# Kernel tuning notes

Measured on AMD Instinct MI355X. Metric: run time of the kernel, lower is better.

Reference implementation:

```python
import jax, jax.numpy as jnp
import numpy as np

T, B, C, H = 2048, 4, 1024, 16
DK = C // H
CLAMP = 1e8  # fp32 clamp bound used by the original module


def setup_inputs() -> dict:
    key = jax.random.key(0)
    ks = jax.random.split(key, 12)
    s = 1.0 / np.sqrt(C)
    inp = {
        'query': jax.random.normal(ks[0], (T, B, C), jnp.float32),
        'key': jax.random.normal(ks[1], (T, B, C), jnp.float32),
        'value': jax.random.normal(ks[2], (T, B, C), jnp.float32),
        'key_padding_mask': jax.random.randint(ks[3], (B, T), 0, 2) > 0,
        # nn.Linear params, stored torch-style as [out, in]
        'Wq': jax.random.uniform(ks[4], (C, C), jnp.float32, -s, s),
        'bq': jax.random.uniform(ks[5], (C,), jnp.float32, -s, s),
        'Wk': jax.random.uniform(ks[6], (C, C), jnp.float32, -s, s),
        'bk': jax.random.uniform(ks[7], (C,), jnp.float32, -s, s),
        'Wv': jax.random.uniform(ks[8], (C, C), jnp.float32, -s, s),
        'bv': jax.random.uniform(ks[9], (C,), jnp.float32, -s, s),
        'Wo': jax.random.uniform(ks[10], (C, C), jnp.float32, -s, s),
        'bo': jax.random.uniform(ks[11], (C,), jnp.float32, -s, s),
    }
    return inp


def _attn(query, key, value, key_padding_mask, Wq, bq, Wk, bk, Wv, bv, Wo, bo):
    # T x B x C -> B x T x C
    q_in = jnp.swapaxes(query, 0, 1)
    k_in = jnp.swapaxes(key, 0, 1)
    v_in = jnp.swapaxes(value, 0, 1)
    b = q_in.shape[0]
    # projections (torch Linear: x @ W.T + b), split heads -> B x H x T x dk
    q = (q_in @ Wq.T + bq).reshape(b, -1, H, DK).transpose(0, 2, 1, 3)
    k = (k_in @ Wk.T + bk).reshape(b, -1, H, DK).transpose(0, 2, 1, 3)
    v = (v_in @ Wv.T + bv).reshape(b, -1, H, DK).transpose(0, 2, 1, 3)
    scores = jnp.einsum('bhqd,bhkd->bhqk', q, k) / np.sqrt(DK)
    if key_padding_mask is not None:
        scores = jnp.where(key_padding_mask[:, None, None, :], -jnp.inf, scores)
    scores = jnp.clip(scores, -CLAMP, CLAMP)
    attn = jax.nn.softmax(scores.astype(jnp.float32), axis=-1).astype(scores.dtype)
    # dropout is identity in eval mode
    x = jnp.einsum('bhqk,bhkd->bhqd', attn, v)
    x = x.transpose(0, 2, 1, 3).reshape(b, -1, H * DK)
    out = x @ Wo.T + bo
    return jnp.swapaxes(out, 0, 1)  # back to T x B x C


def reference(query, key, value, key_padding_mask, Wq, bq, Wk, bk, Wv, bv, Wo, bo):
    return _attn(query, key, value, key_padding_mask, Wq, bq, Wk, bk, Wv, bv, Wo, bo)
```

## Files before the change

kernel.cpp:

```cpp
#include <hip/hip_runtime.h>
#include <hip/hip_bf16.h>
#include <cstddef>
#include <cstdint>

constexpr int T  = 2048;
constexpr int B  = 4;
constexpr int C  = 1024;
constexpr int H  = 16;
constexpr int DK = 64;
constexpr int M  = T * B;

typedef __attribute__((ext_vector_type(8))) short bf16x8;
typedef __attribute__((ext_vector_type(4))) float f32x4;
typedef __attribute__((ext_vector_type(4))) unsigned short u16x4;
typedef __attribute__((ext_vector_type(8))) unsigned short u16x8;

__device__ inline unsigned short f2bf(float f) {
    union { float f; uint32_t u; } v; v.f = f;
    uint32_t u = v.u + 0x7fff + ((v.u >> 16) & 1);
    return (unsigned short)(u >> 16);
}
__device__ inline float bf2f(unsigned short h) {
    union { uint32_t u; float f; } v; v.u = (uint32_t)h << 16;
    return v.f;
}
__device__ inline uint32_t cvtpk_bf16(float lo, float hi) {
    uint32_t r;
    asm("v_cvt_pk_bf16_f32 %0, %1, %2" : "=v"(r) : "v"(lo), "v"(hi));
    return r;
}

__device__ inline void gload_lds16(const void* g, void* l) {
    auto gp = reinterpret_cast<const __attribute__((address_space(1))) char*>(
        reinterpret_cast<uintptr_t>(g));
    auto lp = reinterpret_cast<__attribute__((address_space(3))) char*>(
        reinterpret_cast<uintptr_t>(l));
    __builtin_amdgcn_global_load_lds(gp, lp, 16, 0, 0);
}

__global__ __launch_bounds__(256) void convert_in(const float* __restrict__ q,
                                                  const float* __restrict__ k,
                                                  const float* __restrict__ v,
                                                  unsigned short* __restrict__ dq,
                                                  unsigned short* __restrict__ dk2,
                                                  unsigned short* __restrict__ dv) {
    const float* s; unsigned short* d;
    if (blockIdx.y == 0) { s = q; d = dq; }
    else if (blockIdx.y == 1) { s = k; d = dk2; }
    else { s = v; d = dv; }
    const size_t i = ((size_t)blockIdx.x * 256 + threadIdx.x) * 8;
    const float4 a = *(const float4*)(s + i);
    const float4 b = *(const float4*)(s + i + 4);
    u16x8 o;
    o[0] = f2bf(a.x); o[1] = f2bf(a.y); o[2] = f2bf(a.z); o[3] = f2bf(a.w);
    o[4] = f2bf(b.x); o[5] = f2bf(b.y); o[6] = f2bf(b.z); o[7] = f2bf(b.w);
    *(u16x8*)(d + i) = o;
}

__global__ __launch_bounds__(256) void convert_w(const float* __restrict__ wq,
                                                 const float* __restrict__ wk,
                                                 const float* __restrict__ wv,
                                                 unsigned short* __restrict__ dst) {
    const float* s = blockIdx.y == 0 ? wq : (blockIdx.y == 1 ? wk : wv);
    unsigned short* d = dst + (size_t)blockIdx.y * C * C;
    const size_t i = ((size_t)blockIdx.x * 256 + threadIdx.x) * 8;
    const float4 a = *(const float4*)(s + i);
    const float4 b = *(const float4*)(s + i + 4);
    u16x8 o;
    o[0] = f2bf(a.x); o[1] = f2bf(a.y); o[2] = f2bf(a.z); o[3] = f2bf(a.w);
    o[4] = f2bf(b.x); o[5] = f2bf(b.y); o[6] = f2bf(b.z); o[7] = f2bf(b.w);
    *(u16x8*)(d + i) = o;
}

__global__ __launch_bounds__(256) void convert_wo(const float* __restrict__ wo,
                                                  unsigned short* __restrict__ hi,
                                                  unsigned short* __restrict__ lo) {
    const size_t i = ((size_t)blockIdx.x * 256 + threadIdx.x) * 8;
#pragma unroll
    for (int j = 0; j < 8; j++) {
        const float x = wo[i + j];
        const unsigned short h = f2bf(x);
        hi[i + j] = h;
        lo[i + j] = f2bf(x - bf2f(h));
    }
}

__global__ __launch_bounds__(256) void qkv_gemm(
        const unsigned short* __restrict__ Aq,
        const unsigned short* __restrict__ Ak,
        const unsigned short* __restrict__ Av,
        const unsigned short* __restrict__ W,
        const float* __restrict__ bq, const float* __restrict__ bk,
        const float* __restrict__ bv,
        unsigned short* __restrict__ Qb, unsigned short* __restrict__ Kb,
        unsigned short* __restrict__ Vb) {
    __shared__ __align__(16) unsigned short As[128][32];
    __shared__ __align__(16) unsigned short Ws[128][32];

    const int tid = threadIdx.x;
    const int m0 = blockIdx.x * 128;
    const int n0 = blockIdx.y * 128;
    const int w = tid >> 6, lane = tid & 63;
    const int g = lane >> 4, c16 = lane & 15;
    const int wr = (w >> 1) * 64, wc = (w & 1) * 64;

    const int which = n0 >> 10;
    const unsigned short* A = which == 0 ? Aq : (which == 1 ? Ak : Av);

    f32x4 acc[4][4] = {};

    for (int k0 = 0; k0 < C; k0 += 32) {
        __syncthreads();
#pragma unroll
        for (int half = 0; half < 2; half++) {
            const int chunk = tid + half * 256;
            const int r = chunk >> 2, s = chunk & 3;
            gload_lds16(A + (size_t)(m0 + r) * C + k0 + s * 8,
                        (char*)&As[0][0] + chunk * 16);
            gload_lds16(W + (size_t)(n0 + r) * C + k0 + s * 8,
                        (char*)&Ws[0][0] + chunk * 16);
        }
        __syncthreads();

        bf16x8 af[4], bfr[4];
#pragma unroll
        for (int mf = 0; mf < 4; mf++)
            af[mf] = *(const bf16x8*)&As[wr + mf * 16 + c16][g * 8];
#pragma unroll
        for (int nf = 0; nf < 4; nf++)
            bfr[nf] = *(const bf16x8*)&Ws[wc + nf * 16 + c16][g * 8];
#pragma unroll
        for (int mf = 0; mf < 4; mf++)
#pragma unroll
            for (int nf = 0; nf < 4; nf++)
                acc[mf][nf] = __builtin_amdgcn_mfma_f32_16x16x32_bf16(
                    af[mf], bfr[nf], acc[mf][nf], 0, 0, 0);
    }

    unsigned short* dst = which == 0 ? Qb : (which == 1 ? Kb : Vb);
    const float* bias = which == 0 ? bq : (which == 1 ? bk : bv);
    const float scale = which == 0 ? 0.180336889f : 1.0f;

#pragma unroll
    for (int mf = 0; mf < 4; mf++) {
#pragma unroll
        for (int nf = 0; nf < 4; nf++) {
            const int n = n0 + wc + nf * 16 + c16;
            const int c = n & 1023;
            const int hh = c >> 6, dk = c & 63;
            const float bval = bias[c];
#pragma unroll
            for (int r = 0; r < 4; r++) {
                const int m = m0 + wr + mf * 16 + g * 4 + r;
                const int t = m >> 2, bb = m & 3;
                dst[((size_t)(bb * H + hh) * T + t) * DK + dk] =
                    f2bf((acc[mf][nf][r] + bval) * scale);
            }
        }
    }
}

__global__ __launch_bounds__(256) void oproj_gemm(
        const unsigned short* __restrict__ Xh, const unsigned short* __restrict__ Xl,
        const unsigned short* __restrict__ Wh, const unsigned short* __restrict__ Wl,
        const float* __restrict__ bo, float* __restrict__ out) {
    __shared__ __align__(16) unsigned short Ahs[128][32];
    __shared__ __align__(16) unsigned short Als[128][32];
    __shared__ __align__(16) unsigned short Bhs[128][32];
    __shared__ __align__(16) unsigned short Bls[128][32];

    const int tid = threadIdx.x;
    const int m0 = blockIdx.x * 128;
    const int n0 = blockIdx.y * 128;
    const int w = tid >> 6, lane = tid & 63;
    const int g = lane >> 4, c16 = lane & 15;
    const int wr = (w >> 1) * 64, wc = (w & 1) * 64;

    f32x4 acc[4][4] = {};

    for (int k0 = 0; k0 < C; k0 += 32) {
        __syncthreads();
#pragma unroll
        for (int half = 0; half < 2; half++) {
            const int chunk = tid + half * 256;
            const int r = chunk >> 2, s = chunk & 3;
            const size_t goffA = (size_t)(m0 + r) * C + k0 + s * 8;
            const size_t goffB = (size_t)(n0 + r) * C + k0 + s * 8;
            gload_lds16(Xh + goffA, (char*)&Ahs[0][0] + chunk * 16);
            gload_lds16(Xl + goffA, (char*)&Als[0][0] + chunk * 16);
            gload_lds16(Wh + goffB, (char*)&Bhs[0][0] + chunk * 16);
            gload_lds16(Wl + goffB, (char*)&Bls[0][0] + chunk * 16);
        }
        __syncthreads();

        bf16x8 ah[4], al[4];
#pragma unroll
        for (int mf = 0; mf < 4; mf++) {
            ah[mf] = *(const bf16x8*)&Ahs[wr + mf * 16 + c16][g * 8];
            al[mf] = *(const bf16x8*)&Als[wr + mf * 16 + c16][g * 8];
        }
#pragma unroll
        for (int nf = 0; nf < 4; nf++) {
            const bf16x8 wh = *(const bf16x8*)&Bhs[wc + nf * 16 + c16][g * 8];
            const bf16x8 wl = *(const bf16x8*)&Bls[wc + nf * 16 + c16][g * 8];
#pragma unroll
            for (int mf = 0; mf < 4; mf++) {
                acc[mf][nf] = __builtin_amdgcn_mfma_f32_16x16x32_bf16(ah[mf], wh, acc[mf][nf], 0, 0, 0);
                acc[mf][nf] = __builtin_amdgcn_mfma_f32_16x16x32_bf16(al[mf], wh, acc[mf][nf], 0, 0, 0);
                acc[mf][nf] = __builtin_amdgcn_mfma_f32_16x16x32_bf16(ah[mf], wl, acc[mf][nf], 0, 0, 0);
            }
        }
    }

#pragma unroll
    for (int mf = 0; mf < 4; mf++) {
#pragma unroll
        for (int nf = 0; nf < 4; nf++) {
            const int n = n0 + wc + nf * 16 + c16;
            const float bval = bo[n];
#pragma unroll
            for (int r = 0; r < 4; r++) {
                const int m = m0 + wr + mf * 16 + g * 4 + r;
                const int t = m & 2047, bb = m >> 11;
                out[((size_t)t * B + bb) * C + n] = acc[mf][nf][r] + bval;
            }
        }
    }
}

__global__ __launch_bounds__(256) void attn_mfma(const unsigned short* __restrict__ Q,
                                                 const unsigned short* __restrict__ K,
                                                 const unsigned short* __restrict__ V,
                                                 const int* __restrict__ mask,
                                                 unsigned short* __restrict__ Xh,
                                                 unsigned short* __restrict__ Xl) {
    __shared__ __align__(16) short Ks[64][72];
    __shared__ __align__(16) short Vt[64][72];
    __shared__ __align__(16) short Pl[4][16][72];

    const int b = blockIdx.z, h = blockIdx.y;
    const int q0 = blockIdx.x * 128;
    const int tid = threadIdx.x;
    const int wl = tid >> 6;
    const int lane = tid & 63;
    const int g = lane >> 4;
    const int c16 = lane & 15;

    const size_t bh = (size_t)(b * H + h) * T * DK;
    const unsigned short* Qg = Q + bh;
    const unsigned short* Kg = K + bh;
    const unsigned short* Vg = V + bh;
    const int* mb = mask + b * T;

    bf16x8 qf[2][2];
#pragma unroll
    for (int qs = 0; qs < 2; qs++)
#pragma unroll
        for (int sl = 0; sl < 2; sl++)
            qf[qs][sl] = *(const bf16x8*)(Qg +
                (size_t)(q0 + wl * 32 + qs * 16 + c16) * DK + g * 8 + sl * 32);

    f32x4 o[2][4] = {};
    float lrow[2] = {0.0f, 0.0f};

    for (int kt = 0; kt < T / 64; ++kt) {
        const int kv0 = kt * 64;
        __syncthreads();

#pragma unroll
        for (int i = 0; i < 2; i++) {
            const int chunk = tid + i * 256;
            const int r = chunk >> 3, cc = chunk & 7;
            *(uint4*)&Ks[r][cc * 8] =
                *(const uint4*)(Kg + (size_t)(kv0 + r) * DK + cc * 8);
        }
        {
            const int kp = tid & 31, dc = tid >> 5;
            const u16x8 a0 = *(const u16x8*)(Vg + (size_t)(kv0 + 2 * kp) * DK + dc * 8);
            const u16x8 a1 = *(const u16x8*)(Vg + (size_t)(kv0 + 2 * kp + 1) * DK + dc * 8);
#pragma unroll
            for (int j = 0; j < 8; j++) {
                const uint32_t pk = (uint32_t)a0[j] | ((uint32_t)a1[j] << 16);
                *(uint32_t*)&Vt[dc * 8 + j][2 * kp] = pk;
            }
        }
        __syncthreads();

        const unsigned long long mbits = __ballot(mb[kv0 + lane] != 0);

        bf16x8 kf[4][2], vf[4][2];
#pragma unroll
        for (int t = 0; t < 4; t++)
#pragma unroll
            for (int sl = 0; sl < 2; sl++) {
                kf[t][sl] = *(const bf16x8*)&Ks[t * 16 + c16][g * 8 + sl * 32];
                vf[t][sl] = *(const bf16x8*)&Vt[t * 16 + c16][g * 8 + sl * 32];
            }

#pragma unroll
        for (int qs = 0; qs < 2; qs++) {
            f32x4 s4[4];
#pragma unroll
            for (int t = 0; t < 4; t++) {
                f32x4 acc = {0.f, 0.f, 0.f, 0.f};
#pragma unroll
                for (int sl = 0; sl < 2; sl++)
                    acc = __builtin_amdgcn_mfma_f32_16x16x32_bf16(
                        kf[t][sl], qf[qs][sl], acc, 0, 0, 0);
                s4[t] = acc;
            }

            float rs = 0.0f;
#pragma unroll
            for (int t = 0; t < 4; t++)
#pragma unroll
                for (int r = 0; r < 4; r++) {
                    float p = __builtin_amdgcn_exp2f(s4[t][r]);
                    const int key = 16 * t + 4 * g + r;
                    p = ((mbits >> key) & 1ull) ? 0.0f : p;
                    s4[t][r] = p;
                    rs += p;
                }
            rs += __shfl_xor(rs, 16);
            rs += __shfl_xor(rs, 32);
            lrow[qs] += rs;

#pragma unroll
            for (int t = 0; t < 4; t++)
#pragma unroll
                for (int rr = 0; rr < 2; rr++) {
                    const uint32_t wv = cvtpk_bf16(s4[t][2 * rr], s4[t][2 * rr + 1]);
                    *(uint32_t*)&Pl[wl][c16][16 * t + 4 * g + 2 * rr] = wv;
                }
            bf16x8 pa[2];
#pragma unroll
            for (int sl = 0; sl < 2; sl++)
                pa[sl] = *(const bf16x8*)&Pl[wl][c16][sl * 32 + g * 8];

#pragma unroll
            for (int td = 0; td < 4; td++)
#pragma unroll
                for (int sl = 0; sl < 2; sl++)
                    o[qs][td] = __builtin_amdgcn_mfma_f32_16x16x32_bf16(
                        vf[td][sl], pa[sl], o[qs][td], 0, 0, 0);
        }
    }

#pragma unroll
    for (int qs = 0; qs < 2; qs++) {
        const float inv = 1.0f / lrow[qs];
        const int qq = q0 + wl * 32 + qs * 16 + c16;
#pragma unroll
        for (int td = 0; td < 4; td++) {
            u16x4 hi4, lo4;
#pragma unroll
            for (int r = 0; r < 4; r++) {
                const float val = o[qs][td][r] * inv;
                const unsigned short hv = f2bf(val);
                hi4[r] = hv;
                lo4[r] = f2bf(val - bf2f(hv));
            }
            const size_t idx = ((size_t)b * T + qq) * C + h * DK + td * 16 + 4 * g;
            *(u16x4*)(Xh + idx) = hi4;
            *(u16x4*)(Xl + idx) = lo4;
        }
    }
}

extern "C" void kernel_launch(void* const* d_in, const int* in_sizes, int n_in,
                              void* d_out, int out_size, void* d_ws, size_t ws_size,
                              hipStream_t stream) {
    const float* query = (const float*)d_in[0];
    const float* key   = (const float*)d_in[1];
    const float* value = (const float*)d_in[2];
    const int*   kpm   = (const int*)d_in[3];
    const float* Wq = (const float*)d_in[4];
    const float* bq = (const float*)d_in[5];
    const float* Wk = (const float*)d_in[6];
    const float* bk = (const float*)d_in[7];
    const float* Wv = (const float*)d_in[8];
    const float* bv = (const float*)d_in[9];
    const float* Wo = (const float*)d_in[10];
    const float* bo = (const float*)d_in[11];

    constexpr size_t MB = 1u << 20;
    char* w8 = (char*)d_ws;
    unsigned short* Qa  = (unsigned short*)(w8 + 0 * MB);
    unsigned short* Ka  = (unsigned short*)(w8 + 16 * MB);
    unsigned short* Va  = (unsigned short*)(w8 + 32 * MB);
    unsigned short* WB  = (unsigned short*)(w8 + 48 * MB);
    unsigned short* WoH = (unsigned short*)(w8 + 54 * MB);
    unsigned short* WoL = (unsigned short*)(w8 + 56 * MB);
    unsigned short* Qb  = (unsigned short*)(w8 + 64 * MB);
    unsigned short* Kb  = (unsigned short*)(w8 + 80 * MB);
    unsigned short* Vb  = (unsigned short*)(w8 + 96 * MB);
    unsigned short* XhB = Qa;
    unsigned short* XlB = Ka;

    const dim3 blk(256);

    convert_in<<<dim3(4096, 3), blk, 0, stream>>>(query, key, value, Qa, Ka, Va);
    convert_w<<<dim3(512, 3), blk, 0, stream>>>(Wq, Wk, Wv, WB);
    convert_wo<<<dim3(512, 1), blk, 0, stream>>>(Wo, WoH, WoL);

    qkv_gemm<<<dim3(M / 128, 3 * C / 128), blk, 0, stream>>>(Qa, Ka, Va, WB,
                                                             bq, bk, bv,
                                                             Qb, Kb, Vb);

    attn_mfma<<<dim3(T / 128, H, B), blk, 0, stream>>>(Qb, Kb, Vb, kpm, XhB, XlB);

    oproj_gemm<<<dim3(M / 128, C / 128), blk, 0, stream>>>(XhB, XlB, WoH, WoL,
                                                           bo, (float*)d_out);
}
```

Baseline: 289.6 us.

## Double-buffer K/V tiles in attention with register prefetch and single barrier

The attention kernel now prefetches the next K/V tile and mask word into registers while computing on the current tile, and keeps K and transposed V in double-buffered LDS. That leaves one barrier per iteration instead of two. A custom LDS-only wait-plus-barrier replaces __syncthreads, and compiler fences are added around the per-wave P staging. The goal is to hide global load latency behind the MFMA work, at the cost of more LDS and more registers, which may lower occupancy.

```diff
diff --git a/kernel.cpp b/kernel.cpp
--- a/kernel.cpp
+++ b/kernel.cpp
@@ -9,6 +9,7 @@
 constexpr int H  = 16;
 constexpr int DK = 64;
 constexpr int M  = T * B;
+constexpr int NT = T / 64;
 
 typedef __attribute__((ext_vector_type(8))) short bf16x8;
 typedef __attribute__((ext_vector_type(4))) float f32x4;
@@ -28,6 +29,15 @@
     uint32_t r;
     asm("v_cvt_pk_bf16_f32 %0, %1, %2" : "=v"(r) : "v"(lo), "v"(hi));
     return r;
+}
+__device__ inline void cfence() { asm volatile("" ::: "memory"); }
+
+__device__ inline void block_sync_lds() {
+    __builtin_amdgcn_sched_barrier(0);
+    asm volatile("s_waitcnt lgkmcnt(0)" ::: "memory");
+    __builtin_amdgcn_sched_barrier(0);
+    __builtin_amdgcn_s_barrier();
+    __builtin_amdgcn_sched_barrier(0);
 }
 
 __device__ inline void gload_lds16(const void* g, void* l) {
@@ -234,8 +244,8 @@
                                                  const int* __restrict__ mask,
                                                  unsigned short* __restrict__ Xh,
                                                  unsigned short* __restrict__ Xl) {
-    __shared__ __align__(16) short Ks[64][72];
-    __shared__ __align__(16) short Vt[64][72];
+    __shared__ __align__(16) short Ks[2][64][72];
+    __shared__ __align__(16) short Vt[2][64][72];
     __shared__ __align__(16) short Pl[4][16][72];
 
     const int b = blockIdx.z, h = blockIdx.y;
@@ -263,38 +273,44 @@
     f32x4 o[2][4] = {};
     float lrow[2] = {0.0f, 0.0f};
 
-    for (int kt = 0; kt < T / 64; ++kt) {
-        const int kv0 = kt * 64;
-        __syncthreads();
-
-#pragma unroll
-        for (int i = 0; i < 2; i++) {
-            const int chunk = tid + i * 256;
-            const int r = chunk >> 3, cc = chunk & 7;
-            *(uint4*)&Ks[r][cc * 8] =
-                *(const uint4*)(Kg + (size_t)(kv0 + r) * DK + cc * 8);
-        }
-        {
-            const int kp = tid & 31, dc = tid >> 5;
-            const u16x8 a0 = *(const u16x8*)(Vg + (size_t)(kv0 + 2 * kp) * DK + dc * 8);
-            const u16x8 a1 = *(const u16x8*)(Vg + (size_t)(kv0 + 2 * kp + 1) * DK + dc * 8);
-#pragma unroll
-            for (int j = 0; j < 8; j++) {
-                const uint32_t pk = (uint32_t)a0[j] | ((uint32_t)a1[j] << 16);
-                *(uint32_t*)&Vt[dc * 8 + j][2 * kp] = pk;
-            }
-        }
-        __syncthreads();
-
-        const unsigned long long mbits = __ballot(mb[kv0 + lane] != 0);
+    const int skr = tid >> 3;
+    const int skc = (tid & 7) * 8;
+    const int kp = tid & 31, dc = tid >> 5;
+    uint4 kra, krb; u16x8 va, vb; int mw;
+
+#define ISSUE(kv0)                                                              \
+    do {                                                                        \
+        kra = *(const uint4*)(Kg + (size_t)((kv0) + skr) * DK + skc);           \
+        krb = *(const uint4*)(Kg + (size_t)((kv0) + skr + 32) * DK + skc);      \
+        va  = *(const u16x8*)(Vg + (size_t)((kv0) + 2 * kp) * DK + dc * 8);     \
+        vb  = *(const u16x8*)(Vg + (size_t)((kv0) + 2 * kp + 1) * DK + dc * 8); \
+        mw  = mb[(kv0) + lane];                                                 \
+    } while (0)
+
+    ISSUE(0);
+
+    for (int kt = 0; kt < NT; ++kt) {
+        const int buf = kt & 1;
+
+        const unsigned long long mbits = __ballot(mw != 0);
+        *(uint4*)&Ks[buf][skr][skc] = kra;
+        *(uint4*)&Ks[buf][skr + 32][skc] = krb;
+#pragma unroll
+        for (int j = 0; j < 8; j++) {
+            *(uint32_t*)&Vt[buf][dc * 8 + j][2 * kp] =
+                (uint32_t)(unsigned short)va[j] | ((uint32_t)(unsigned short)vb[j] << 16);
+        }
+        if (kt + 1 < NT) ISSUE((kt + 1) * 64);
+
+        block_sync_lds();
 
         bf16x8 kf[4][2], vf[4][2];
 #pragma unroll
         for (int t = 0; t < 4; t++)
 #pragma unroll
             for (int sl = 0; sl < 2; sl++) {
-                kf[t][sl] = *(const bf16x8*)&Ks[t * 16 + c16][g * 8 + sl * 32];
-                vf[t][sl] = *(const bf16x8*)&Vt[t * 16 + c16][g * 8 + sl * 32];
+                kf[t][sl] = *(const bf16x8*)&Ks[buf][t * 16 + c16][g * 8 + sl * 32];
+                vf[t][sl] = *(const bf16x8*)&Vt[buf][t * 16 + c16][g * 8 + sl * 32];
             }
 
 #pragma unroll
@@ -303,10 +319,8 @@
 #pragma unroll
             for (int t = 0; t < 4; t++) {
                 f32x4 acc = {0.f, 0.f, 0.f, 0.f};
-#pragma unroll
-                for (int sl = 0; sl < 2; sl++)
-                    acc = __builtin_amdgcn_mfma_f32_16x16x32_bf16(
-                        kf[t][sl], qf[qs][sl], acc, 0, 0, 0);
+                acc = __builtin_amdgcn_mfma_f32_16x16x32_bf16(kf[t][0], qf[qs][0], acc, 0, 0, 0);
+                acc = __builtin_amdgcn_mfma_f32_16x16x32_bf16(kf[t][1], qf[qs][1], acc, 0, 0, 0);
                 s4[t] = acc;
             }
 
@@ -325,6 +339,7 @@
             rs += __shfl_xor(rs, 32);
             lrow[qs] += rs;
 
+            cfence();
 #pragma unroll
             for (int t = 0; t < 4; t++)
 #pragma unroll
@@ -332,19 +347,20 @@
                     const uint32_t wv = cvtpk_bf16(s4[t][2 * rr], s4[t][2 * rr + 1]);
                     *(uint32_t*)&Pl[wl][c16][16 * t + 4 * g + 2 * rr] = wv;
                 }
+            cfence();
             bf16x8 pa[2];
-#pragma unroll
-            for (int sl = 0; sl < 2; sl++)
-                pa[sl] = *(const bf16x8*)&Pl[wl][c16][sl * 32 + g * 8];
-
-#pragma unroll
-            for (int td = 0; td < 4; td++)
-#pragma unroll
-                for (int sl = 0; sl < 2; sl++)
-                    o[qs][td] = __builtin_amdgcn_mfma_f32_16x16x32_bf16(
-                        vf[td][sl], pa[sl], o[qs][td], 0, 0, 0);
-        }
-    }
+            pa[0] = *(const bf16x8*)&Pl[wl][c16][g * 8];
+            pa[1] = *(const bf16x8*)&Pl[wl][c16][g * 8 + 32];
+            cfence();
+
+#pragma unroll
+            for (int td = 0; td < 4; td++) {
+                o[qs][td] = __builtin_amdgcn_mfma_f32_16x16x32_bf16(vf[td][0], pa[0], o[qs][td], 0, 0, 0);
+                o[qs][td] = __builtin_amdgcn_mfma_f32_16x16x32_bf16(vf[td][1], pa[1], o[qs][td], 0, 0, 0);
+            }
+        }
+    }
+#undef ISSUE
 
 #pragma unroll
     for (int qs = 0; qs < 2; qs++) {
```

Result: faster. 273.1 us (-5.7%).
